# Performance work log

Hardware: AMD Instinct MI355X
Metric: run time of the kernel (lower is better)

## Reference

```python
import jax, jax.numpy as jnp
import numpy as np
from jax import lax

DN = ('NHWC', 'HWIO', 'NHWC')


def conv_same(x, w):
    return lax.conv_general_dilated(x, w, window_strides=(1, 1), padding='SAME',
                                    dimension_numbers=DN)


def dwconv(x, w):
    # w: (kh, kw, F, 1) TF depthwise layout -> HWIO (kh, kw, 1, F), groups=F
    F = w.shape[2]
    return lax.conv_general_dilated(x, jnp.transpose(w, (0, 1, 3, 2)),
                                    window_strides=(1, 1), padding='SAME',
                                    dimension_numbers=DN, feature_group_count=F)


def hard_sigmoid(x):
    return jnp.clip(0.2 * x + 0.5, 0.0, 1.0)


def setup_inputs() -> dict:
    key = jax.random.key(0)
    ks = jax.random.split(key, 10)
    B, H, W, Cin, F = 16, 128, 128, 64, 64
    s = 0.05
    return {
        'inputs': jax.random.normal(ks[0], (B, H, W, Cin), jnp.float32),
        'h0': jax.random.normal(ks[1], (B, H, W, F), jnp.float32),
        'c0': jax.random.normal(ks[2], (B, H, W, F), jnp.float32),
        'm0': jax.random.normal(ks[3], (B, H, W, F), jnp.float32),
        'kernel': jax.random.normal(ks[4], (3, 3, Cin, 4 * F), jnp.float32) * s,
        'recurrent_kernel': jax.random.normal(ks[5], (3, 3, F, 4 * F), jnp.float32) * s,
        'bias': jnp.concatenate([jnp.zeros((F,), jnp.float32),
                                 jnp.ones((F,), jnp.float32),
                                 jnp.zeros((2 * F,), jnp.float32)]),
        'sa_kernel': jax.random.normal(ks[6], (1, 1, F, 5), jnp.float32) * s,
        'kernel_z': jax.random.normal(ks[7], (3, 3, 2, F), jnp.float32) * s,
        'depth_wise_kernel': jax.random.normal(ks[8], (3, 3, F, 6), jnp.float32) * s,
        'sa_bias': jnp.zeros((3 * F,), jnp.float32),
    }


def reference(inputs, h0, c0, m0, kernel, recurrent_kernel, bias, sa_kernel,
              kernel_z, depth_wise_kernel, sa_bias):
    F = h0.shape[-1]
    # --- ConvLSTM gates (no dropout: all four gates share the same input, so
    # a single fused conv over the 4F-channel kernel is the same math) ---
    xz = conv_same(inputs, kernel) + bias  # [B,H,W,4F]
    hz = conv_same(h0, recurrent_kernel)   # [B,H,W,4F]
    z = xz + hz
    zi_, zf_, zc_, zo_ = jnp.split(z, 4, axis=-1)
    i = hard_sigmoid(zi_)
    f = hard_sigmoid(zf_)
    c = f * c0 + i * jnp.tanh(zc_)
    o = hard_sigmoid(zo_)
    h = o * jnp.tanh(c)  # [B,H,W,F]

    # --- Self-attention memory (SAM) module; 1x1 convs -> channel contractions ---
    w = sa_kernel[0, 0]  # [F,5]
    v_h = jnp.einsum('bhwc,c->bhw', h, w[:, 0])
    k_h = jnp.einsum('bhwc,c->bhw', h, w[:, 1])
    q_h = jnp.einsum('bhwc,c->bhw', h, w[:, 2])
    k_m = jnp.einsum('bhwc,c->bhw', m0, w[:, 3])
    v_m = jnp.einsum('bhwc,c->bhw', m0, w[:, 4])

    alpha_m = jax.nn.softmax(jnp.matmul(q_h, k_m), axis=-1)  # [B,H,H] (H==W)
    alpha_h = jax.nn.softmax(jnp.matmul(q_h, k_h), axis=-1)
    z_m = jnp.matmul(alpha_m, v_m)  # [B,H,W]
    z_h = jnp.matmul(alpha_h, v_h)

    zi = conv_same(jnp.stack([z_h, z_m], axis=-1), kernel_z)  # [B,H,W,F]

    dw = depth_wise_kernel  # [3,3,F,6]
    b_i, b_g, b_o = jnp.split(sa_bias, 3)
    i2 = jax.nn.sigmoid(dwconv(zi, dw[..., 0:1]) + dwconv(h, dw[..., 1:2]) + b_i)
    g = jnp.tanh(dwconv(zi, dw[..., 2:3]) + dwconv(h, dw[..., 3:4]) + b_g)
    o2 = jax.nn.sigmoid(dwconv(zi, dw[..., 4:5]) + dwconv(h, dw[..., 5:6]) + b_o)

    m_t = (1.0 - i2) * m0 + i2 * g
    h_hat = m_t * o2
    return h_hat, c, m_t
```

## Files before the change

### kernel.cpp

```cpp
#include <hip/hip_runtime.h>

#define BB 16
#define HH 128
#define WW 128
#define FF 64
#define NPIX (BB*HH*WW)

typedef short bf16x8 __attribute__((ext_vector_type(8)));
typedef float f32x4 __attribute__((ext_vector_type(4)));

__device__ __forceinline__ float bf2f(unsigned int u){ return __uint_as_float(u<<16); }
__device__ __forceinline__ unsigned short f2bf(float f){
  unsigned u = __float_as_uint(f);
  u += 0x7fffu + ((u>>16)&1u);
  return (unsigned short)(u>>16);
}
__device__ __forceinline__ float hsig(float x){ return fminf(fmaxf(fmaf(0.2f,x,0.5f),0.f),1.f); }
__device__ __forceinline__ float tanh_fast(float x){
  float e = __expf(2.f*x);
  return 1.f - 2.f/(e + 1.f);
}
__device__ __forceinline__ void gload_lds16(const void* g, void* l){
  __builtin_amdgcn_global_load_lds(
      (const __attribute__((address_space(1))) unsigned int*)g,
      (__attribute__((address_space(3))) unsigned int*)l, 16, 0, 0);
}

__global__ __launch_bounds__(256) void zero_pads(unsigned short* __restrict__ Xp){
  int i = blockIdx.x*256 + threadIdx.x;
  if (i >= 16*516) return;
  int b = i / 516, r = i % 516;
  int y, x;
  if (r < 130){ y = 0; x = r; }
  else if (r < 260){ y = 129; x = r-130; }
  else if (r < 388){ y = r-260+1; x = 0; }
  else { y = r-388+1; x = 129; }
  unsigned short* p = Xp + (((size_t)(b*130 + y)*130) + x)*128;
  uint4 z = {0u,0u,0u,0u};
  #pragma unroll
  for (int c=0;c<16;++c) ((uint4*)p)[c] = z;
}

__global__ __launch_bounds__(256) void prep_x(const float* __restrict__ in,
                                              const float* __restrict__ h0,
                                              unsigned short* __restrict__ Xp){
  int gi = blockIdx.x*256 + threadIdx.x;
  int pix = gi >> 4;
  int ch8 = (gi & 15) * 8;
  const float* src = (ch8 < 64) ? (in + (size_t)pix*64 + ch8)
                                : (h0 + (size_t)pix*64 + (ch8-64));
  float4 v0 = *(const float4*)src;
  float4 v1 = *(const float4*)(src+4);
  uint4 o;
  o.x = (unsigned)f2bf(v0.x) | ((unsigned)f2bf(v0.y)<<16);
  o.y = (unsigned)f2bf(v0.z) | ((unsigned)f2bf(v0.w)<<16);
  o.z = (unsigned)f2bf(v1.x) | ((unsigned)f2bf(v1.y)<<16);
  o.w = (unsigned)f2bf(v1.z) | ((unsigned)f2bf(v1.w)<<16);
  int b = pix >> 14, y = (pix >> 7) & 127, x = pix & 127;
  *(uint4*)(Xp + (((size_t)(b*130 + y+1)*130) + (x+1))*128 + ch8) = o;
}

__global__ __launch_bounds__(256) void prep_w(const float* __restrict__ kern,
                                              const float* __restrict__ rkern,
                                              unsigned short* __restrict__ Wg){
  int k = blockIdx.x;
  int n = threadIdx.x;
  int tap = k >> 7, c = k & 127;
  float v = (c < 64) ? kern[((size_t)(tap*64 + c))*256 + n]
                     : rkern[((size_t)(tap*64 + (c-64)))*256 + n];
  Wg[(size_t)n*1152 + k] = f2bf(v);
}

__global__ __launch_bounds__(256, 2) void gates_kernel(
    const unsigned short* __restrict__ Xp,
    const unsigned short* __restrict__ Wg,
    const float* __restrict__ bias,
    const float* __restrict__ c0,
    float* __restrict__ c_out,
    unsigned short* __restrict__ h_bf){
  __shared__ unsigned short As[2][130*128];
  const int gid = blockIdx.x;
  const int swz = (gid & 7)*256 + (gid >> 3);
  const int b  = swz >> 7;
  const int y  = swz & 127;
  const int tid = threadIdx.x;
  const int l = tid & 63;
  const int wid = tid >> 6;
  const int l15 = l & 15, l4 = l >> 4;
  const int n0 = wid*16 + l15;

  const unsigned short* brow[4];
  #pragma unroll
  for (int g=0; g<4; ++g) brow[g] = Wg + (size_t)(g*64 + n0)*1152 + l4*8;

  f32x4 acc[8][4];
  #pragma unroll
  for (int mf=0;mf<8;++mf)
    #pragma unroll
    for (int g=0;g<4;++g) acc[mf][g] = (f32x4){0.f,0.f,0.f,0.f};

  auto stage = [&](int buf, int dyi){
    const unsigned short* gbase = Xp + ((size_t)((b*130 + y + dyi)*130))*128;
    unsigned short* lbase = &As[buf][0];
    #pragma unroll
    for (int it=0; it<8; ++it){
      int q = it*256 + tid;
      int px = q >> 4, c = q & 15;
      int cs = c ^ (px & 7);
      gload_lds16(gbase + (size_t)px*128 + cs*8, lbase + (size_t)q*8);
    }
    if (l < 8){
      int q = 2048 + wid*8 + l;
      int px = q >> 4, c = q & 15;
      int cs = c ^ (px & 7);
      gload_lds16(gbase + (size_t)px*128 + cs*8, lbase + (size_t)q*8);
    }
  };

  stage(0, 0);
  for (int dyi = 0; dyi < 3; ++dyi){
    if (dyi < 2){
      stage((dyi+1)&1, dyi+1);
      asm volatile("s_waitcnt vmcnt(9)" ::: "memory");
    } else {
      asm volatile("s_waitcnt vmcnt(0)" ::: "memory");
    }
    __builtin_amdgcn_sched_barrier(0);
    __builtin_amdgcn_s_barrier();
    __builtin_amdgcn_sched_barrier(0);
    const unsigned short* asb = &As[dyi&1][0];
    #pragma unroll
    for (int dxi = 0; dxi < 3; ++dxi){
      const int tap = dyi*3 + dxi;
      #pragma unroll
      for (int ksc = 0; ksc < 2; ++ksc){
        bf16x8 bfr[4][2];
        #pragma unroll
        for (int g=0; g<4; ++g)
          #pragma unroll
          for (int k2=0; k2<2; ++k2)
            bfr[g][k2] = *(const bf16x8*)(brow[g] + tap*128 + (ksc*2+k2)*32);
        #pragma unroll
        for (int k2=0; k2<2; ++k2){
          const int cd = (ksc*2+k2)*4 + l4;
          #pragma unroll
          for (int mf=0; mf<8; ++mf){
            const int px = mf*16 + l15 + dxi;
            bf16x8 a = *(const bf16x8*)(asb + (size_t)px*128 + ((cd ^ (px & 7))*8));
            #pragma unroll
            for (int g=0;g<4;++g)
              acc[mf][g] = __builtin_amdgcn_mfma_f32_16x16x32_bf16(a, bfr[g][k2], acc[mf][g], 0,0,0);
          }
        }
      }
    }
    __builtin_amdgcn_sched_barrier(0);
    __builtin_amdgcn_s_barrier();
    __builtin_amdgcn_sched_barrier(0);
  }
  const float b0 = bias[n0], b1 = bias[64+n0], b2 = bias[128+n0], b3 = bias[192+n0];
  const size_t prow = (size_t)(b*128 + y)*128;
  #pragma unroll
  for (int mf=0;mf<8;++mf){
    #pragma unroll
    for (int r=0;r<4;++r){
      const int x = mf*16 + l4*4 + r;
      const size_t p = prow + x;
      const float zi_ = acc[mf][0][r] + b0;
      const float zf_ = acc[mf][1][r] + b1;
      const float zc_ = acc[mf][2][r] + b2;
      const float zo_ = acc[mf][3][r] + b3;
      const float iv = hsig(zi_), fv = hsig(zf_), ov = hsig(zo_);
      const float cv = fv*c0[p*64 + n0] + iv*tanh_fast(zc_);
      const float hv = ov*tanh_fast(cv);
      c_out[p*64 + n0] = cv;
      h_bf[p*64 + n0] = f2bf(hv);
    }
  }
}

__global__ __launch_bounds__(256) void qkv_kernel(
    const unsigned short* __restrict__ h_bf, const float* __restrict__ m0,
    const float* __restrict__ sak,
    float* __restrict__ q_h, float* __restrict__ k_h, float* __restrict__ v_h,
    float* __restrict__ k_m, float* __restrict__ v_m){
  __shared__ float wS[320];
  for (int i = threadIdx.x; i < 320; i += 256) wS[i] = sak[i];
  __syncthreads();
  const int p = blockIdx.x*256 + threadIdx.x;
  const unsigned short* hp = h_bf + (size_t)p*64;
  const float* mp = m0 + (size_t)p*64;
  float a0=0,a1=0,a2=0,a3=0,a4=0;
  #pragma unroll
  for (int ch = 0; ch < 64; ch += 8){
    uint4 hu = *(const uint4*)(hp + ch);
    float4 ma = *(const float4*)(mp + ch);
    float4 mb = *(const float4*)(mp + ch + 4);
    float hv[8] = { bf2f(hu.x&0xffffu), bf2f(hu.x>>16), bf2f(hu.y&0xffffu), bf2f(hu.y>>16),
                    bf2f(hu.z&0xffffu), bf2f(hu.z>>16), bf2f(hu.w&0xffffu), bf2f(hu.w>>16) };
    float mv[8] = { ma.x,ma.y,ma.z,ma.w, mb.x,mb.y,mb.z,mb.w };
    #pragma unroll
    for (int jj=0;jj<8;++jj){
      const float* w = &wS[(ch+jj)*5];
      a0 = fmaf(hv[jj], w[0], a0);
      a1 = fmaf(hv[jj], w[1], a1);
      a2 = fmaf(hv[jj], w[2], a2);
      a3 = fmaf(mv[jj], w[3], a3);
      a4 = fmaf(mv[jj], w[4], a4);
    }
  }
  v_h[p]=a0; k_h[p]=a1; q_h[p]=a2; k_m[p]=a3; v_m[p]=a4;
}

__global__ __launch_bounds__(256) void attn_kernel(
    const float* __restrict__ q_h, const float* __restrict__ k_h, const float* __restrict__ v_h,
    const float* __restrict__ k_m, const float* __restrict__ v_m,
    float* __restrict__ z_h, float* __restrict__ z_m){
  __shared__ float q2[2][128];
  __shared__ float al[2][128];
  __shared__ float redm[2][2], reds[2][2];
  const int bid = blockIdx.x;
  const int b = bid >> 5;
  const int type = (bid >> 4) & 1;
  const int rb = bid & 15;
  const float* K = (type ? k_m : k_h) + (size_t)b*16384;
  const float* V = (type ? v_m : v_h) + (size_t)b*16384;
  const float* Q = q_h + (size_t)b*16384;
  float* Z = (type ? z_m : z_h) + (size_t)b*16384;
  const int t = threadIdx.x, rg = t>>7, j = t&127, lane = t&63, hw = (t>>6)&1;
  for (int it = 0; it < 4; ++it){
    const int i = rb*8 + it*2 + rg;
    __syncthreads();
    q2[rg][j] = Q[i*128 + j];
    __syncthreads();
    float s0=0.f, s1=0.f, s2=0.f, s3=0.f;
    #pragma unroll
    for (int w=0; w<128; w+=4){
      s0 = fmaf(q2[rg][w  ], K[(w  )*128 + j], s0);
      s1 = fmaf(q2[rg][w+1], K[(w+1)*128 + j], s1);
      s2 = fmaf(q2[rg][w+2], K[(w+2)*128 + j], s2);
      s3 = fmaf(q2[rg][w+3], K[(w+3)*128 + j], s3);
    }
    float s = (s0+s1)+(s2+s3);
    float mx = s;
    #pragma unroll
    for (int o=1;o<64;o<<=1) mx = fmaxf(mx, __shfl_xor(mx, o));
    if (lane==0) redm[rg][hw] = mx;
    __syncthreads();
    mx = fmaxf(redm[rg][0], redm[rg][1]);
    float pe = __expf(s - mx);
    float sm = pe;
    #pragma unroll
    for (int o=1;o<64;o<<=1) sm += __shfl_xor(sm, o);
    if (lane==0) reds[rg][hw] = sm;
    __syncthreads();
    const float inv = 1.f/(reds[rg][0]+reds[rg][1]);
    al[rg][j] = pe*inv;
    __syncthreads();
    float z0=0.f, z1=0.f, z2=0.f, z3=0.f;
    #pragma unroll
    for (int w=0; w<128; w+=4){
      z0 = fmaf(al[rg][w  ], V[(w  )*128 + j], z0);
      z1 = fmaf(al[rg][w+1], V[(w+1)*128 + j], z1);
      z2 = fmaf(al[rg][w+2], V[(w+2)*128 + j], z2);
      z3 = fmaf(al[rg][w+3], V[(w+3)*128 + j], z3);
    }
    Z[i*128 + j] = (z0+z1)+(z2+z3);
  }
}

__global__ __launch_bounds__(512) void final_fused(
    const float* __restrict__ z_h, const float* __restrict__ z_m,
    const float* __restrict__ kz,
    const unsigned short* __restrict__ h_bf,
    const float* __restrict__ m0, const float* __restrict__ dwk,
    const float* __restrict__ sab,
    float* __restrict__ hhat, float* __restrict__ m_t){
  __shared__ unsigned short zi[4][128][64];
  const int f = threadIdx.x & 63;
  const int g = threadIdx.x >> 6;
  const int blk = blockIdx.x;
  const int b = blk >> 6;
  const int y0 = (blk & 63) * 2;

  {
    const int ry = g >> 1;
    const int xh = g & 1;
    const int yy = y0 - 1 + ry;
    const int x0 = xh * 64;
    if ((unsigned)yy >= 128u){
      for (int i=0;i<64;++i) zi[ry][x0+i][f] = 0;
    } else {
      float w0[9], w1[9];
      #pragma unroll
      for (int tap=0; tap<9; ++tap){
        w0[tap] = kz[tap*128 + f];
        w1[tap] = kz[tap*128 + 64 + f];
      }
      const float* zhr = z_h + (size_t)(b*128 + yy)*128;
      const float* zmr = z_m + (size_t)(b*128 + yy)*128;
      const bool ym = (yy > 0), yp = (yy < 127);
      float az[3][3], am[3][3];
      auto ldc = [&](int x, float (&Z)[3], float (&M)[3]){
        if ((unsigned)x < 128u){
          Z[0] = ym ? zhr[x-128] : 0.f;  M[0] = ym ? zmr[x-128] : 0.f;
          Z[1] = zhr[x];                 M[1] = zmr[x];
          Z[2] = yp ? zhr[x+128] : 0.f;  M[2] = yp ? zmr[x+128] : 0.f;
        } else { Z[0]=Z[1]=Z[2]=0.f; M[0]=M[1]=M[2]=0.f; }
      };
      ldc(x0-1, az[0], am[0]);
      ldc(x0,   az[1], am[1]);
      for (int i=0; i<64; ++i){
        const int x = x0 + i;
        ldc(x+1, az[2], am[2]);
        float acc = 0.f;
        #pragma unroll
        for (int tap=0; tap<9; ++tap){
          const int dy = tap/3, dx = tap%3;
          acc = fmaf(az[dx][dy], w0[tap], acc);
          acc = fmaf(am[dx][dy], w1[tap], acc);
        }
        zi[ry][x][f] = f2bf(acc);
        #pragma unroll
        for (int k=0;k<3;++k){
          az[0][k]=az[1][k]; az[1][k]=az[2][k];
          am[0][k]=am[1][k]; am[1][k]=am[2][k];
        }
      }
    }
  }
  __syncthreads();

  const int r2 = g >> 2;
  const int xq = g & 3;
  const int y = y0 + r2;
  const size_t rb = (size_t)(b*128 + y)*128;
  float wv[9][6];
  #pragma unroll
  for (int tap=0;tap<9;++tap)
    #pragma unroll
    for (int jj=0;jj<6;++jj) wv[tap][jj] = dwk[(tap*64 + f)*6 + jj];
  const float bi = sab[f], bg = sab[64+f], bo = sab[128+f];
  const bool ym = (y > 0), yp = (y < 127);
  float vz[3][3], vh[3][3];
  auto ldc2 = [&](int x, float (&Z)[3], float (&H)[3]){
    if ((unsigned)x < 128u){
      const size_t base = (rb + x)*64 + f;
      H[0] = ym ? bf2f(h_bf[base - 8192]) : 0.f;
      H[1] = bf2f(h_bf[base]);
      H[2] = yp ? bf2f(h_bf[base + 8192]) : 0.f;
      Z[0] = bf2f(zi[r2  ][x][f]);
      Z[1] = bf2f(zi[r2+1][x][f]);
      Z[2] = bf2f(zi[r2+2][x][f]);
    } else { Z[0]=Z[1]=Z[2]=0.f; H[0]=H[1]=H[2]=0.f; }
  };
  const int x0 = xq*32;
  ldc2(x0-1, vz[0], vh[0]);
  ldc2(x0,   vz[1], vh[1]);
  for (int i=0; i<32; ++i){
    const int x = x0 + i;
    ldc2(x+1, vz[2], vh[2]);
    float si=0.f, sg=0.f, so=0.f;
    #pragma unroll
    for (int tap=0;tap<9;++tap){
      const int dy = tap/3, dx = tap%3;
      const float zv = vz[dx][dy], hv = vh[dx][dy];
      si = fmaf(zv, wv[tap][0], si); si = fmaf(hv, wv[tap][1], si);
      sg = fmaf(zv, wv[tap][2], sg); sg = fmaf(hv, wv[tap][3], sg);
      so = fmaf(zv, wv[tap][4], so); so = fmaf(hv, wv[tap][5], so);
    }
    const size_t p = rb + x;
    const float i2 = 1.f/(1.f+__expf(-(si+bi)));
    const float gg = tanh_fast(sg+bg);
    const float o2 = 1.f/(1.f+__expf(-(so+bo)));
    const float mv = m0[p*64+f];
    const float mt = (1.f-i2)*mv + i2*gg;
    hhat[p*64+f] = mt*o2;
    m_t[p*64+f]  = mt;
    #pragma unroll
    for (int k=0;k<3;++k){
      vz[0][k]=vz[1][k]; vz[1][k]=vz[2][k];
      vh[0][k]=vh[1][k]; vh[1][k]=vh[2][k];
    }
  }
}

extern "C" void kernel_launch(void* const* d_in, const int* in_sizes, int n_in,
                              void* d_out, int out_size, void* d_ws, size_t ws_size,
                              hipStream_t stream){
  const float* inputs = (const float*)d_in[0];
  const float* h0p    = (const float*)d_in[1];
  const float* c0p    = (const float*)d_in[2];
  const float* m0p    = (const float*)d_in[3];
  const float* kern   = (const float*)d_in[4];
  const float* rkern  = (const float*)d_in[5];
  const float* biasp  = (const float*)d_in[6];
  const float* sakp   = (const float*)d_in[7];
  const float* kzp    = (const float*)d_in[8];
  const float* dwkp   = (const float*)d_in[9];
  const float* sabp   = (const float*)d_in[10];
  float* out = (float*)d_out;
  char* ws = (char*)d_ws;

  constexpr size_t SZ_XP  = (size_t)16*130*130*128*2;
  constexpr size_t SZ_WG  = (size_t)256*1152*2;
  constexpr size_t SZ_HBF = (size_t)NPIX*64*2;
  constexpr size_t SZA    = (size_t)NPIX*4;
  constexpr size_t OFF_XP  = 0;
  constexpr size_t OFF_WG  = OFF_XP + SZ_XP;
  constexpr size_t OFF_HBF = OFF_WG + SZ_WG;
  constexpr size_t OFF_Q   = OFF_HBF + SZ_HBF;
  constexpr size_t OFF_KH  = OFF_Q  + SZA;
  constexpr size_t OFF_VH  = OFF_KH + SZA;
  constexpr size_t OFF_KM  = OFF_VH + SZA;
  constexpr size_t OFF_VM  = OFF_KM + SZA;
  constexpr size_t OFF_ZH  = OFF_VM + SZA;
  constexpr size_t OFF_ZM  = OFF_ZH + SZA;

  unsigned short* Xp  = (unsigned short*)(ws + OFF_XP);
  unsigned short* Wg  = (unsigned short*)(ws + OFF_WG);
  unsigned short* Hbf = (unsigned short*)(ws + OFF_HBF);
  float* Qh = (float*)(ws + OFF_Q);
  float* Kh = (float*)(ws + OFF_KH);
  float* Vh = (float*)(ws + OFF_VH);
  float* Km = (float*)(ws + OFF_KM);
  float* Vm = (float*)(ws + OFF_VM);
  float* Zh = (float*)(ws + OFF_ZH);
  float* Zm = (float*)(ws + OFF_ZM);

  zero_pads<<<33, 256, 0, stream>>>(Xp);
  prep_x<<<NPIX*16/256, 256, 0, stream>>>(inputs, h0p, Xp);
  prep_w<<<1152, 256, 0, stream>>>(kern, rkern, Wg);
  gates_kernel<<<2048, 256, 0, stream>>>(Xp, Wg, biasp, c0p,
                                         out + (size_t)NPIX*64, Hbf);
  qkv_kernel<<<NPIX/256, 256, 0, stream>>>(Hbf, m0p, sakp, Qh, Kh, Vh, Km, Vm);
  attn_kernel<<<512, 256, 0, stream>>>(Qh, Kh, Vh, Km, Vm, Zh, Zm);
  final_fused<<<1024, 512, 0, stream>>>(Zh, Zm, kzp, Hbf, m0p, dwkp, sabp,
                                        out, out + 2*(size_t)NPIX*64);
}
```

Measured before the change: 420.8 us.

## Stage K and V in shared memory and register-tile attention rows

The attention kernel now loads each batch's full K and V matrices into LDS once per block and computes 16 query rows per block, with each thread producing four adjacent output columns via float4 LDS reads. Softmax reductions stay within a 32-lane group, so the cross-wave LDS reductions and extra barriers are gone. The goal is to stop re-reading K and V from global memory for every row. In exchange the grid is halved to 256 blocks and each block uses about 140KB of LDS, which limits occupancy to one block per CU.

```diff
diff --git a/kernel.cpp b/kernel.cpp
--- a/kernel.cpp
+++ b/kernel.cpp
@@ -216,56 +216,65 @@
     const float* __restrict__ q_h, const float* __restrict__ k_h, const float* __restrict__ v_h,
     const float* __restrict__ k_m, const float* __restrict__ v_m,
     float* __restrict__ z_h, float* __restrict__ z_m){
-  __shared__ float q2[2][128];
-  __shared__ float al[2][128];
-  __shared__ float redm[2][2], reds[2][2];
+  __shared__ float Kl[128][132];
+  __shared__ float Vl[128][132];
+  __shared__ float q2[8][132];
+  __shared__ float al[8][132];
   const int bid = blockIdx.x;
-  const int b = bid >> 5;
-  const int type = (bid >> 4) & 1;
-  const int rb = bid & 15;
+  const int b = bid >> 4;
+  const int type = (bid >> 3) & 1;
+  const int rb = bid & 7;
   const float* K = (type ? k_m : k_h) + (size_t)b*16384;
   const float* V = (type ? v_m : v_h) + (size_t)b*16384;
   const float* Q = q_h + (size_t)b*16384;
   float* Z = (type ? z_m : z_h) + (size_t)b*16384;
-  const int t = threadIdx.x, rg = t>>7, j = t&127, lane = t&63, hw = (t>>6)&1;
-  for (int it = 0; it < 4; ++it){
-    const int i = rb*8 + it*2 + rg;
+  const int t = threadIdx.x;
+  const int jq = t & 31;
+  const int r8 = t >> 5;
+
+  for (int base = 0; base < 16384; base += 1024){
+    const int idx = base + t*4;
+    const int w = idx >> 7, j = idx & 127;
+    const float4 kv = *(const float4*)(K + idx);
+    const float4 vv = *(const float4*)(V + idx);
+    *(float4*)&Kl[w][j] = kv;
+    *(float4*)&Vl[w][j] = vv;
+  }
+
+  for (int p = 0; p < 2; ++p){
     __syncthreads();
-    q2[rg][j] = Q[i*128 + j];
+    for (int idx = t; idx < 1024; idx += 256)
+      q2[idx>>7][idx&127] = Q[(rb*16 + p*8 + (idx>>7))*128 + (idx&127)];
     __syncthreads();
-    float s0=0.f, s1=0.f, s2=0.f, s3=0.f;
-    #pragma unroll
-    for (int w=0; w<128; w+=4){
-      s0 = fmaf(q2[rg][w  ], K[(w  )*128 + j], s0);
-      s1 = fmaf(q2[rg][w+1], K[(w+1)*128 + j], s1);
-      s2 = fmaf(q2[rg][w+2], K[(w+2)*128 + j], s2);
-      s3 = fmaf(q2[rg][w+3], K[(w+3)*128 + j], s3);
-    }
-    float s = (s0+s1)+(s2+s3);
-    float mx = s;
-    #pragma unroll
-    for (int o=1;o<64;o<<=1) mx = fmaxf(mx, __shfl_xor(mx, o));
-    if (lane==0) redm[rg][hw] = mx;
+    const int i = rb*16 + p*8 + r8;
+    float s0=0.f,s1=0.f,s2=0.f,s3=0.f;
+    #pragma unroll 8
+    for (int w=0; w<128; ++w){
+      const float qv = q2[r8][w];
+      const float4 kv = *(const float4*)&Kl[w][jq*4];
+      s0 = fmaf(qv, kv.x, s0); s1 = fmaf(qv, kv.y, s1);
+      s2 = fmaf(qv, kv.z, s2); s3 = fmaf(qv, kv.w, s3);
+    }
+    float mx = fmaxf(fmaxf(s0,s1), fmaxf(s2,s3));
+    #pragma unroll
+    for (int o=1;o<32;o<<=1) mx = fmaxf(mx, __shfl_xor(mx, o));
+    const float p0 = __expf(s0-mx), p1 = __expf(s1-mx);
+    const float p2 = __expf(s2-mx), p3 = __expf(s3-mx);
+    float sm = (p0+p1)+(p2+p3);
+    #pragma unroll
+    for (int o=1;o<32;o<<=1) sm += __shfl_xor(sm, o);
+    const float inv = 1.f/sm;
+    *(float4*)&al[r8][jq*4] = make_float4(p0*inv, p1*inv, p2*inv, p3*inv);
     __syncthreads();
-    mx = fmaxf(redm[rg][0], redm[rg][1]);
-    float pe = __expf(s - mx);
-    float sm = pe;
-    #pragma unroll
-    for (int o=1;o<64;o<<=1) sm += __shfl_xor(sm, o);
-    if (lane==0) reds[rg][hw] = sm;
-    __syncthreads();
-    const float inv = 1.f/(reds[rg][0]+reds[rg][1]);
-    al[rg][j] = pe*inv;
-    __syncthreads();
-    float z0=0.f, z1=0.f, z2=0.f, z3=0.f;
-    #pragma unroll
-    for (int w=0; w<128; w+=4){
-      z0 = fmaf(al[rg][w  ], V[(w  )*128 + j], z0);
-      z1 = fmaf(al[rg][w+1], V[(w+1)*128 + j], z1);
-      z2 = fmaf(al[rg][w+2], V[(w+2)*128 + j], z2);
-      z3 = fmaf(al[rg][w+3], V[(w+3)*128 + j], z3);
-    }
-    Z[i*128 + j] = (z0+z1)+(z2+z3);
+    float z0=0.f,z1=0.f,z2=0.f,z3=0.f;
+    #pragma unroll 8
+    for (int w=0; w<128; ++w){
+      const float av = al[r8][w];
+      const float4 vv = *(const float4*)&Vl[w][jq*4];
+      z0 = fmaf(av, vv.x, z0); z1 = fmaf(av, vv.y, z1);
+      z2 = fmaf(av, vv.z, z2); z3 = fmaf(av, vv.w, z3);
+    }
+    *(float4*)(Z + (size_t)i*128 + jq*4) = make_float4(z0,z1,z2,z3);
   }
 }
 
@@ -434,7 +443,7 @@
   gates_kernel<<<2048, 256, 0, stream>>>(Xp, Wg, biasp, c0p,
                                          out + (size_t)NPIX*64, Hbf);
   qkv_kernel<<<NPIX/256, 256, 0, stream>>>(Hbf, m0p, sakp, Qh, Kh, Vh, Km, Vm);
-  attn_kernel<<<512, 256, 0, stream>>>(Qh, Kh, Vh, Km, Vm, Zh, Zm);
+  attn_kernel<<<256, 256, 0, stream>>>(Qh, Kh, Vh, Km, Vm, Zh, Zm);
   final_fused<<<1024, 512, 0, stream>>>(Zh, Zm, kzp, Hbf, m0p, dwkp, sabp,
                                         out, out + 2*(size_t)NPIX*64);
 }
```

After: 409.4 us. 1.03x faster.
